# Kernel optimization log

Measured on AMD Instinct MI355X. Metric: run time of the kernel, lower is better.

Reference implementation:

```python
import jax, jax.numpy as jnp
import numpy as np

B, T, D, K = 16, 8192, 64, 1024


def setup_inputs() -> dict:
    key = jax.random.key(0)
    k1, k2 = jax.random.split(key)
    x = jax.random.normal(k1, (B, T, D, 1), dtype=jnp.float32)
    weight = jax.random.normal(k2, (K, D), dtype=jnp.float32)
    return {"x": x, "weight": weight}


def reference(x, weight):
    # x: [B, T, D, 1] -> squeeze trailing dim -> [B, T, D]
    xs = jnp.squeeze(x, axis=-1)
    x2 = jnp.sum(xs * xs, axis=-1, keepdims=True)          # [B, T, 1]
    e2 = jnp.sum(weight * weight, axis=-1)                 # [K]
    xe = jnp.einsum('btd,kd->btk', xs, weight)             # [B, T, K]
    dist2 = x2 - 2.0 * xe + e2                             # [B, T, K]
    indices = jnp.argmin(dist2, axis=-1)                   # [B, T] int
    quantized = jnp.take(weight, indices, axis=0)          # [B, T, D]
    return quantized, indices
```

## Files before the change

kernel.cpp:

```cpp
#include <hip/hip_runtime.h>

#define MTOK  131072
#define DIMD  64
#define KCODE 1024
#define TPB   256
#define CHK   128
#define NCHK  8
#define CBPC  8

typedef __bf16 bf16x8 __attribute__((ext_vector_type(8)));
typedef float  f32x4  __attribute__((ext_vector_type(4)));

__device__ __forceinline__ f32x4 mfma16(bf16x8 a, bf16x8 b, f32x4 c) {
    return __builtin_amdgcn_mfma_f32_16x16x32_bf16(a, b, c, 0, 0, 0);
}

__device__ __forceinline__ void g2l16(const void* g, void* l) {
    __builtin_amdgcn_global_load_lds(
        (const __attribute__((address_space(1))) unsigned int*)g,
        (__attribute__((address_space(3))) unsigned int*)l, 16, 0, 0);
}

__global__ __launch_bounds__(256) void prep_kernel(
    const float* __restrict__ w, __bf16* __restrict__ wpk,
    float* __restrict__ e2n, float* __restrict__ e2) {
    int cb  = blockIdx.x;
    int tid = threadIdx.x;
    int win = tid >> 6, lane = tid & 63;
    int q = lane >> 4, m = lane & 15;
    int k = cb * 16 + m;
    int d0 = (win & 1) * 32 + q * 8;
    const float* src = w + (size_t)k * DIMD + d0;
    float4 v0 = *(const float4*)(src);
    float4 v1 = *(const float4*)(src + 4);
    float f[8] = {v0.x, v0.y, v0.z, v0.w, v1.x, v1.y, v1.z, v1.w};
    bf16x8 o;
#pragma unroll
    for (int j = 0; j < 8; ++j) {
        __bf16 h = (__bf16)f[j];
        o[j] = (win < 2) ? h : (__bf16)(f[j] - (float)h);
    }
    *(bf16x8*)(wpk + ((size_t)(cb * 4 + win) * 64 + lane) * 8) = o;

    if (tid < 16) {
        int k2 = cb * 16 + tid;
        const float4* row = (const float4*)(w + (size_t)k2 * DIMD);
        float s = 0.f;
#pragma unroll
        for (int i = 0; i < 16; ++i) {
            float4 v = row[i];
            s = fmaf(v.x, v.x, s); s = fmaf(v.y, v.y, s);
            s = fmaf(v.z, v.z, s); s = fmaf(v.w, v.w, s);
        }
        e2[k2]  = s;
        e2n[k2] = -0.5f * s;
    }
}

__global__ __launch_bounds__(256, 2) void vq_main(
    const float* __restrict__ x, const float* __restrict__ wfull,
    const __bf16* __restrict__ wpk, const float* __restrict__ e2n_g,
    const float* __restrict__ e2_g, float* __restrict__ out) {

    __shared__ __align__(16) __bf16 ldsW[2][CBPC * 4 * 64 * 8];
    __shared__ __align__(16) float  ldsE[KCODE];
    __shared__ int   ldsIdx[TPB];
    __shared__ int   flist[TPB];
    __shared__ float redV[256];
    __shared__ int   redI[256];
    __shared__ int   nflag;

    const int tid  = threadIdx.x;
    const int blk  = blockIdx.x;
    const int lane = tid & 63;
    const int wv   = tid >> 6;
    const int q    = lane >> 4;
    const int m    = lane & 15;

    {
        const char* gsrc = (const char*)wpk + (size_t)wv * 8192 + (size_t)lane * 16;
        char* ldst = (char*)&ldsW[0][0] + wv * 8192 + lane * 16;
#pragma unroll
        for (int j = 0; j < 8; ++j)
            g2l16(gsrc + j * 1024, ldst + j * 1024);
    }
    ((f32x4*)ldsE)[tid] = ((const f32x4*)e2n_g)[tid];
    if (tid == 0) nflag = 0;

    bf16x8 bx[4][4];
#pragma unroll
    for (int tg = 0; tg < 4; ++tg) {
        const float* xr = x + ((size_t)blk * TPB + wv * 64 + tg * 16 + m) * DIMD;
#pragma unroll
        for (int h = 0; h < 2; ++h) {
            float4 v0 = *(const float4*)(xr + h * 32 + q * 8);
            float4 v1 = *(const float4*)(xr + h * 32 + q * 8 + 4);
            float f[8] = {v0.x, v0.y, v0.z, v0.w, v1.x, v1.y, v1.z, v1.w};
            bf16x8 hi, lo;
#pragma unroll
            for (int j = 0; j < 8; ++j) {
                __bf16 hh = (__bf16)f[j];
                hi[j] = hh;
                lo[j] = (__bf16)(f[j] - (float)hh);
            }
            bx[tg][h]     = hi;
            bx[tg][2 + h] = lo;
        }
    }

    float b1[4], b2[4]; int i1[4];
#pragma unroll
    for (int tg = 0; tg < 4; ++tg) { b1[tg] = -3e38f; b2[tg] = -3e38f; i1[tg] = 0; }

    __syncthreads();

    for (int ck = 0; ck < NCHK; ++ck) {
        if (ck + 1 < NCHK) {
            const char* gsrc = (const char*)wpk + (size_t)(ck + 1) * 32768
                             + (size_t)wv * 8192 + (size_t)lane * 16;
            char* ldst = (char*)&ldsW[(ck + 1) & 1][0] + wv * 8192 + lane * 16;
#pragma unroll
            for (int j = 0; j < 8; ++j)
                g2l16(gsrc + j * 1024, ldst + j * 1024);
        }
        const __bf16* wb = &ldsW[ck & 1][0];
#pragma unroll
        for (int cb = 0; cb < CBPC; ++cb) {
            bf16x8 a0 = *(const bf16x8*)(wb + (size_t)(cb * 4 + 0) * 512 + lane * 8);
            bf16x8 a1 = *(const bf16x8*)(wb + (size_t)(cb * 4 + 1) * 512 + lane * 8);
            bf16x8 a2 = *(const bf16x8*)(wb + (size_t)(cb * 4 + 2) * 512 + lane * 8);
            bf16x8 a3 = *(const bf16x8*)(wb + (size_t)(cb * 4 + 3) * 512 + lane * 8);
            f32x4 e = *(const f32x4*)&ldsE[ck * CHK + cb * 16 + q * 4];
            int base = ck * CHK + cb * 16 + q * 4;
#pragma unroll
            for (int tg = 0; tg < 4; ++tg) {
                f32x4 t = e;
                t = mfma16(a0, bx[tg][0], t);
                t = mfma16(a1, bx[tg][1], t);
                t = mfma16(a0, bx[tg][2], t);
                t = mfma16(a1, bx[tg][3], t);
                t = mfma16(a2, bx[tg][0], t);
                t = mfma16(a3, bx[tg][1], t);
#pragma unroll
                for (int r = 0; r < 4; ++r) {
                    float a  = t[r];
                    int idxv = base + r;
                    bool gt  = a > b1[tg];
                    i1[tg] = gt ? idxv : i1[tg];
                    b2[tg] = __builtin_amdgcn_fmed3f(a, b1[tg], b2[tg]);
                    b1[tg] = fmaxf(a, b1[tg]);
                }
            }
        }
        __syncthreads();
    }

#pragma unroll
    for (int tg = 0; tg < 4; ++tg) {
        float B1 = b1[tg], B2 = b2[tg]; int I1 = i1[tg];
#pragma unroll
        for (int mask = 16; mask <= 32; mask <<= 1) {
            float ob1 = __shfl_xor(B1, mask);
            float ob2 = __shfl_xor(B2, mask);
            int   oi  = __shfl_xor(I1, mask);
            bool take = (ob1 > B1) || (ob1 == B1 && oi < I1);
            B2 = fmaxf(fminf(ob1, B1), fmaxf(ob2, B2));
            I1 = take ? oi : I1;
            B1 = fmaxf(ob1, B1);
        }
        if (q == 0) {
            int tl = wv * 64 + tg * 16 + m;
            ldsIdx[tl] = I1;
            if (B1 - B2 < 2e-3f) { int p = atomicAdd(&nflag, 1); flist[p] = tl; }
        }
    }
    __syncthreads();

    int nf = nflag;
    for (int f = 0; f < nf; ++f) {
        int tl = flist[f];
        const float4* xr = (const float4*)(x + (size_t)(blk * TPB + tl) * DIMD);
        float bv = 3e38f; int bi = 0;
#pragma unroll
        for (int j = 0; j < 4; ++j) {
            int k = tid * 4 + j;
            const float4* wr = (const float4*)(wfull + (size_t)k * DIMD);
            float s = 0.f;
#pragma unroll
            for (int i = 0; i < 16; ++i) {
                float4 xv = xr[i];
                float4 wv4 = wr[i];
                s = fmaf(xv.x, wv4.x, s); s = fmaf(xv.y, wv4.y, s);
                s = fmaf(xv.z, wv4.z, s); s = fmaf(xv.w, wv4.w, s);
            }
            float dv = fmaf(-2.f, s, e2_g[k]);
            if (dv < bv) { bv = dv; bi = k; }
        }
        redV[tid] = bv; redI[tid] = bi;
        __syncthreads();
        if (tid == 0) {
            float v = redV[0]; int b = redI[0];
            for (int t2 = 1; t2 < 256; ++t2)
                if (redV[t2] < v) { v = redV[t2]; b = redI[t2]; }
            ldsIdx[tl] = b;
        }
        __syncthreads();
    }

    out[(size_t)MTOK * DIMD + (size_t)blk * TPB + tid] = (float)ldsIdx[tid];
    {
        int gi = ldsIdx[tid];
        const float4* wr = (const float4*)(wfull + (size_t)gi * DIMD);
        float4* o = (float4*)(out + ((size_t)blk * TPB + tid) * DIMD);
#pragma unroll
        for (int j = 0; j < 16; ++j) o[j] = wr[j];
    }
}

extern "C" void kernel_launch(void* const* d_in, const int* in_sizes, int n_in,
                              void* d_out, int out_size, void* d_ws, size_t ws_size,
                              hipStream_t stream) {
    const float* x = (const float*)d_in[0];
    const float* w = (const float*)d_in[1];
    float* out = (float*)d_out;

    __bf16* wpk = (__bf16*)d_ws;
    float*  e2n = (float*)((char*)d_ws + 262144);
    float*  e2  = (float*)((char*)d_ws + 266240);

    prep_kernel<<<64, 256, 0, stream>>>(w, wpk, e2n, e2);
    vq_main<<<MTOK / TPB, 256, 0, stream>>>(x, w, wpk, e2n, e2, out);
}
```

Before: 174.7 us.

## Drop LDS staging; read packed codebook from global with register double-buffering

Removes the LDS double-buffered codebook staging and all block-level barriers. Each wave now loads its codebook fragments straight from global (L2/L1-cached) memory, with a two-deep register prefetch. The near-tie refinement is now done per wave with ballot and shuffle reductions instead of block-wide LDS lists and serial reductions. This is meant to remove __syncthreads stalls and LDS traffic and to let waves progress on their own. In exchange, every wave issues redundant global loads of the same codebook, and the loop leans on cache hit rates and on hiding load latency.

Result: faster. 162.8 us (-6.8%).

```diff
diff --git a/kernel.cpp b/kernel.cpp
--- a/kernel.cpp
+++ b/kernel.cpp
@@ -4,21 +4,12 @@
 #define DIMD  64
 #define KCODE 1024
 #define TPB   256
-#define CHK   128
-#define NCHK  8
-#define CBPC  8
 
 typedef __bf16 bf16x8 __attribute__((ext_vector_type(8)));
 typedef float  f32x4  __attribute__((ext_vector_type(4)));
 
 __device__ __forceinline__ f32x4 mfma16(bf16x8 a, bf16x8 b, f32x4 c) {
     return __builtin_amdgcn_mfma_f32_16x16x32_bf16(a, b, c, 0, 0, 0);
-}
-
-__device__ __forceinline__ void g2l16(const void* g, void* l) {
-    __builtin_amdgcn_global_load_lds(
-        (const __attribute__((address_space(1))) unsigned int*)g,
-        (__attribute__((address_space(3))) unsigned int*)l, 16, 0, 0);
 }
 
 __global__ __launch_bounds__(256) void prep_kernel(
@@ -62,14 +53,6 @@
     const __bf16* __restrict__ wpk, const float* __restrict__ e2n_g,
     const float* __restrict__ e2_g, float* __restrict__ out) {
 
-    __shared__ __align__(16) __bf16 ldsW[2][CBPC * 4 * 64 * 8];
-    __shared__ __align__(16) float  ldsE[KCODE];
-    __shared__ int   ldsIdx[TPB];
-    __shared__ int   flist[TPB];
-    __shared__ float redV[256];
-    __shared__ int   redI[256];
-    __shared__ int   nflag;
-
     const int tid  = threadIdx.x;
     const int blk  = blockIdx.x;
     const int lane = tid & 63;
@@ -77,16 +60,6 @@
     const int q    = lane >> 4;
     const int m    = lane & 15;
 
-    {
-        const char* gsrc = (const char*)wpk + (size_t)wv * 8192 + (size_t)lane * 16;
-        char* ldst = (char*)&ldsW[0][0] + wv * 8192 + lane * 16;
-#pragma unroll
-        for (int j = 0; j < 8; ++j)
-            g2l16(gsrc + j * 1024, ldst + j * 1024);
-    }
-    ((f32x4*)ldsE)[tid] = ((const f32x4*)e2n_g)[tid];
-    if (tid == 0) nflag = 0;
-
     bf16x8 bx[4][4];
 #pragma unroll
     for (int tg = 0; tg < 4; ++tg) {
@@ -112,49 +85,57 @@
 #pragma unroll
     for (int tg = 0; tg < 4; ++tg) { b1[tg] = -3e38f; b2[tg] = -3e38f; i1[tg] = 0; }
 
-    __syncthreads();
-
-    for (int ck = 0; ck < NCHK; ++ck) {
-        if (ck + 1 < NCHK) {
-            const char* gsrc = (const char*)wpk + (size_t)(ck + 1) * 32768
-                             + (size_t)wv * 8192 + (size_t)lane * 16;
-            char* ldst = (char*)&ldsW[(ck + 1) & 1][0] + wv * 8192 + lane * 16;
-#pragma unroll
-            for (int j = 0; j < 8; ++j)
-                g2l16(gsrc + j * 1024, ldst + j * 1024);
-        }
-        const __bf16* wb = &ldsW[ck & 1][0];
-#pragma unroll
-        for (int cb = 0; cb < CBPC; ++cb) {
-            bf16x8 a0 = *(const bf16x8*)(wb + (size_t)(cb * 4 + 0) * 512 + lane * 8);
-            bf16x8 a1 = *(const bf16x8*)(wb + (size_t)(cb * 4 + 1) * 512 + lane * 8);
-            bf16x8 a2 = *(const bf16x8*)(wb + (size_t)(cb * 4 + 2) * 512 + lane * 8);
-            bf16x8 a3 = *(const bf16x8*)(wb + (size_t)(cb * 4 + 3) * 512 + lane * 8);
-            f32x4 e = *(const f32x4*)&ldsE[ck * CHK + cb * 16 + q * 4];
-            int base = ck * CHK + cb * 16 + q * 4;
-#pragma unroll
-            for (int tg = 0; tg < 4; ++tg) {
-                f32x4 t = e;
-                t = mfma16(a0, bx[tg][0], t);
-                t = mfma16(a1, bx[tg][1], t);
-                t = mfma16(a0, bx[tg][2], t);
-                t = mfma16(a1, bx[tg][3], t);
-                t = mfma16(a2, bx[tg][0], t);
-                t = mfma16(a3, bx[tg][1], t);
-#pragma unroll
-                for (int r = 0; r < 4; ++r) {
-                    float a  = t[r];
-                    int idxv = base + r;
-                    bool gt  = a > b1[tg];
-                    i1[tg] = gt ? idxv : i1[tg];
-                    b2[tg] = __builtin_amdgcn_fmed3f(a, b1[tg], b2[tg]);
-                    b1[tg] = fmaxf(a, b1[tg]);
-                }
-            }
-        }
-        __syncthreads();
-    }
-
+    auto step = [&](bf16x8 f0, bf16x8 f1, bf16x8 f2, bf16x8 f3, f32x4 ee, int cbase) {
+#pragma unroll
+        for (int tg = 0; tg < 4; ++tg) {
+            f32x4 t = mfma16(f0, bx[tg][0], ee);
+            t = mfma16(f1, bx[tg][1], t);
+            t = mfma16(f0, bx[tg][2], t);
+            t = mfma16(f1, bx[tg][3], t);
+            t = mfma16(f2, bx[tg][0], t);
+            t = mfma16(f3, bx[tg][1], t);
+#pragma unroll
+            for (int r = 0; r < 4; ++r) {
+                float a   = t[r];
+                int idxv  = cbase + q * 4 + r;
+                bool gt   = a > b1[tg];
+                i1[tg] = gt ? idxv : i1[tg];
+                b2[tg] = __builtin_amdgcn_fmed3f(a, b1[tg], b2[tg]);
+                b1[tg] = fmaxf(a, b1[tg]);
+            }
+        }
+    };
+
+    const __bf16* wb = wpk + lane * 8;
+    const float*  eb = e2n_g + q * 4;
+    bf16x8 A0 = *(const bf16x8*)(wb + 0);
+    bf16x8 A1 = *(const bf16x8*)(wb + 512);
+    bf16x8 A2 = *(const bf16x8*)(wb + 1024);
+    bf16x8 A3 = *(const bf16x8*)(wb + 1536);
+    f32x4  EA = *(const f32x4*)(eb);
+
+    for (int cb = 0; cb < 64; cb += 2) {
+        const __bf16* pB = wb + (size_t)(cb + 1) * 2048;
+        bf16x8 B0 = *(const bf16x8*)(pB + 0);
+        bf16x8 B1 = *(const bf16x8*)(pB + 512);
+        bf16x8 B2 = *(const bf16x8*)(pB + 1024);
+        bf16x8 B3 = *(const bf16x8*)(pB + 1536);
+        f32x4  EB = *(const f32x4*)(eb + (cb + 1) * 16);
+
+        step(A0, A1, A2, A3, EA, cb * 16);
+
+        if (cb + 2 < 64) {
+            const __bf16* pA = wb + (size_t)(cb + 2) * 2048;
+            A0 = *(const bf16x8*)(pA + 0);
+            A1 = *(const bf16x8*)(pA + 512);
+            A2 = *(const bf16x8*)(pA + 1024);
+            A3 = *(const bf16x8*)(pA + 1536);
+            EA = *(const f32x4*)(eb + (cb + 2) * 16);
+        }
+        step(B0, B1, B2, B3, EB, (cb + 1) * 16);
+    }
+
+    float B1f[4], B2f[4]; int I1f[4];
 #pragma unroll
     for (int tg = 0; tg < 4; ++tg) {
         float B1 = b1[tg], B2 = b2[tg]; int I1 = i1[tg];
@@ -168,50 +149,58 @@
             I1 = take ? oi : I1;
             B1 = fmaxf(ob1, B1);
         }
-        if (q == 0) {
-            int tl = wv * 64 + tg * 16 + m;
-            ldsIdx[tl] = I1;
-            if (B1 - B2 < 2e-3f) { int p = atomicAdd(&nflag, 1); flist[p] = tl; }
-        }
-    }
-    __syncthreads();
-
-    int nf = nflag;
-    for (int f = 0; f < nf; ++f) {
-        int tl = flist[f];
-        const float4* xr = (const float4*)(x + (size_t)(blk * TPB + tl) * DIMD);
-        float bv = 3e38f; int bi = 0;
-#pragma unroll
-        for (int j = 0; j < 4; ++j) {
-            int k = tid * 4 + j;
-            const float4* wr = (const float4*)(wfull + (size_t)k * DIMD);
-            float s = 0.f;
-#pragma unroll
-            for (int i = 0; i < 16; ++i) {
-                float4 xv = xr[i];
-                float4 wv4 = wr[i];
-                s = fmaf(xv.x, wv4.x, s); s = fmaf(xv.y, wv4.y, s);
-                s = fmaf(xv.z, wv4.z, s); s = fmaf(xv.w, wv4.w, s);
-            }
-            float dv = fmaf(-2.f, s, e2_g[k]);
-            if (dv < bv) { bv = dv; bi = k; }
-        }
-        redV[tid] = bv; redI[tid] = bi;
-        __syncthreads();
-        if (tid == 0) {
-            float v = redV[0]; int b = redI[0];
-            for (int t2 = 1; t2 < 256; ++t2)
-                if (redV[t2] < v) { v = redV[t2]; b = redI[t2]; }
-            ldsIdx[tl] = b;
-        }
-        __syncthreads();
-    }
-
-    out[(size_t)MTOK * DIMD + (size_t)blk * TPB + tid] = (float)ldsIdx[tid];
+        B1f[tg] = B1; B2f[tg] = B2; I1f[tg] = I1;
+    }
+
+    int myidx;
     {
-        int gi = ldsIdx[tid];
-        const float4* wr = (const float4*)(wfull + (size_t)gi * DIMD);
-        float4* o = (float4*)(out + ((size_t)blk * TPB + tid) * DIMD);
+        int src = lane & 15;
+        int v0 = __shfl(I1f[0], src);
+        int v1 = __shfl(I1f[1], src);
+        int v2 = __shfl(I1f[2], src);
+        int v3 = __shfl(I1f[3], src);
+        int tg4 = lane >> 4;
+        myidx = (tg4 == 0) ? v0 : (tg4 == 1) ? v1 : (tg4 == 2) ? v2 : v3;
+    }
+
+    for (int tg = 0; tg < 4; ++tg) {
+        unsigned long long msk =
+            __ballot((lane < 16) && (B1f[tg] - B2f[tg] < 2e-3f));
+        while (msk) {
+            int mm = __ffsll((unsigned long long)msk) - 1;
+            msk &= msk - 1;
+            int tloc = tg * 16 + mm;
+            const float4* xr = (const float4*)(x + ((size_t)blk * TPB + wv * 64 + tloc) * DIMD);
+            float bv = 3e38f; int bi = 0;
+            for (int j = 0; j < 16; ++j) {
+                int k = lane * 16 + j;
+                const float4* wr = (const float4*)(wfull + (size_t)k * DIMD);
+                float s = 0.f;
+#pragma unroll
+                for (int i = 0; i < 16; ++i) {
+                    float4 xv = xr[i], wv4 = wr[i];
+                    s = fmaf(xv.x, wv4.x, s); s = fmaf(xv.y, wv4.y, s);
+                    s = fmaf(xv.z, wv4.z, s); s = fmaf(xv.w, wv4.w, s);
+                }
+                float dv = fmaf(-2.f, s, e2_g[k]);
+                if (dv < bv) { bv = dv; bi = k; }
+            }
+#pragma unroll
+            for (int mask2 = 1; mask2 <= 32; mask2 <<= 1) {
+                float ov = __shfl_xor(bv, mask2);
+                int   oi = __shfl_xor(bi, mask2);
+                bool take = (ov < bv) || (ov == bv && oi < bi);
+                bv = take ? ov : bv;
+                bi = take ? oi : bi;
+            }
+            myidx = (lane == tloc) ? bi : myidx;
+        }
+    }
+
+    out[(size_t)MTOK * DIMD + (size_t)blk * TPB + wv * 64 + lane] = (float)myidx;
+    {
+        const float4* wr = (const float4*)(wfull + (size_t)myidx * DIMD);
+        float4* o = (float4*)(out + ((size_t)blk * TPB + wv * 64 + lane) * DIMD);
 #pragma unroll
         for (int j = 0; j < 16; ++j) o[j] = wr[j];
     }
```
